# Kernel optimization log

Hardware: AMD Instinct MI355X
Metric: run time of the kernel (lower is better)

The kernel has to match this reference:

```python
import jax, jax.numpy as jnp
import numpy as np

B, C, N = 8, 256, 2048
NMOD = 5  # time, space, time_cor, space_cor, global_res


def _attn(x, y, Wqk, Vw, Vb, Tw, Tb):
    """Offset self-attention (PCT-style). x, y: [B, C, N].
    q/k share the same 1x1-conv weight Wqk; v and trans convs have bias.
    softmax over last axis, then L1 renorm over axis=1 of the [B,N,N] map.
    """
    x_q = jnp.einsum('oc,bcn->bno', Wqk, y)           # [B,N,C]
    x_k = jnp.einsum('oc,bcn->bon', Wqk, x)           # [B,C,N]
    x_v = jnp.einsum('oc,bcn->bon', Vw, x) + Vb[:, None]
    att = jax.nn.softmax(jnp.einsum('bnc,bcm->bnm', x_q, x_k), axis=-1)
    att = att / (1e-07 + att.sum(axis=1, keepdims=True))
    x_r = jnp.einsum('bcn,bnm->bcm', x_v, att)        # [B,C,N]
    x_r = jax.nn.relu(jnp.einsum('oc,bcn->bon', Tw, x - x_r) + Tb[:, None])
    return x + x_r


def setup_inputs() -> dict:
    key = jax.random.key(0)
    ks = jax.random.split(key, 6)
    s = 1.0 / np.sqrt(C)
    return {
        'x':   jax.random.normal(ks[0], (B, 3, C, N), dtype=jnp.float32),
        'Wqk': jax.random.normal(ks[1], (NMOD, C, C), dtype=jnp.float32) * s,
        'Vw':  jax.random.normal(ks[2], (NMOD, C, C), dtype=jnp.float32) * s,
        'Vb':  jax.random.normal(ks[3], (NMOD, C), dtype=jnp.float32) * s,
        'Tw':  jax.random.normal(ks[4], (NMOD, C, C), dtype=jnp.float32) * s,
        'Tb':  jax.random.normal(ks[5], (NMOD, C), dtype=jnp.float32) * s,
    }


def reference(x, Wqk, Vw, Vb, Tw, Tb):
    time_x, mid, space_x = x[:, 0], x[:, 1], x[:, 2]

    def A(i, xx, yy):
        return _attn(xx, yy, Wqk[i], Vw[i], Vb[i], Tw[i], Tb[i])

    time_att = A(0, time_x, time_x)
    space_att = A(1, space_x, space_x)
    time_cor = A(2, time_x, space_x)
    space_cor = A(3, space_x, time_x)
    global_feat = A(4, mid, mid)

    time_update = jnp.tanh(time_att * jax.nn.sigmoid(time_cor))
    space_update = jnp.tanh(space_att * jax.nn.sigmoid(space_cor))
    g_sig = jax.nn.sigmoid(global_feat)
    global_residual = jax.nn.sigmoid(time_update * g_sig + space_update * g_sig)
    return mid + global_residual * jnp.tanh(global_feat)
```

## Files before the change

kernel.cpp:

```cpp
#include <hip/hip_runtime.h>
#include <math.h>

#define BB 8
#define CC 256
#define NN 2048

static const size_t NC  = (size_t)NN * CC;
static const size_t CN  = (size_t)CC * NN;
static const size_t XBS = 3 * CN;

typedef unsigned short u16;
typedef __attribute__((ext_vector_type(8))) short short8;
typedef __attribute__((ext_vector_type(4))) float f32x4;

__device__ __forceinline__ float bf2f(u16 v) {
    union { unsigned int u; float f; } t; t.u = ((unsigned int)v) << 16; return t.f;
}
__device__ __forceinline__ u16 f2bf(float f) {
    union { float f; unsigned int u; } t; t.f = f;
    return (u16)((t.u + 0x7fffu + ((t.u >> 16) & 1u)) >> 16);
}
__device__ __forceinline__ float sigf(float x) { return 1.0f / (1.0f + expf(-x)); }

__device__ __forceinline__ size_t til(int r, int c, int tpr) {
    return (((size_t)((r >> 4) * tpr + (c >> 5))) << 9)
         + (size_t)((r & 15) << 5) + (size_t)(c & 31);
}

__global__ __launch_bounds__(256) void cast_w(const float* __restrict__ in,
                                              u16* __restrict__ outp)
{
    const int mat = blockIdx.y;
    const int idx = blockIdx.x * 256 + threadIdx.x;
    const int c = idx >> 6, k = (idx & 63) << 2;
    const float4 v = *(const float4*)&in[(size_t)mat * (CC * CC) + (size_t)c * CC + k];
    ushort4 p;
    p.x = f2bf(v.x); p.y = f2bf(v.y); p.z = f2bf(v.z); p.w = f2bf(v.w);
    *(ushort4*)&outp[(size_t)mat * (CC * CC) + til(c, k, CC / 32)] = p;
}

__global__ __launch_bounds__(256) void tcast_x(const float* __restrict__ in,
                                               u16* __restrict__ out)
{
    const int z = blockIdx.z;
    const float* I = in + (size_t)z * CN;
    u16* O = out + (size_t)z * NC;
    const int c0 = blockIdx.y * 64, n0 = blockIdx.x * 64;
    const int tx = threadIdx.x & 15, ty = threadIdx.x >> 4;

    __shared__ float t[64][68];

    #pragma unroll
    for (int cc = 0; cc < 64; cc += 16) {
        const int c = ty + cc;
        *(float4*)&t[c][tx * 4] = *(const float4*)&I[(size_t)(c0 + c) * NN + n0 + tx * 4];
    }
    __syncthreads();
    #pragma unroll
    for (int nn2 = 0; nn2 < 64; nn2 += 16) {
        const int n = n0 + ty + nn2;
        const int c = c0 + tx * 4;
        ushort4 p;
        p.x = f2bf(t[tx * 4 + 0][ty + nn2]);
        p.y = f2bf(t[tx * 4 + 1][ty + nn2]);
        p.z = f2bf(t[tx * 4 + 2][ty + nn2]);
        p.w = f2bf(t[tx * 4 + 3][ty + nn2]);
        *(ushort4*)&O[til(n, c, 8)] = p;
    }
}

struct QkvP {
    const u16* w[12]; const u16* x[12]; u16* out[12];
    const float* bias[12]; int isv[12];
};

__global__ __launch_bounds__(256) void conv_qkv(QkvP P)
{
    const int z = blockIdx.z, job = z >> 3, b = z & 7;
    const int isv = P.isv[job];
    const u16* Wp = P.w[job];
    const u16* Xp = P.x[job] + (size_t)b * (3 * NC);
    const int n0 = blockIdx.x * 128, c0 = blockIdx.y * 128;
    const int lane = threadIdx.x & 63, wave = threadIdx.x >> 6;
    const int l15 = lane & 15, lg = lane >> 4;
    const int rA = (wave >> 1) * 64, rB = (wave & 1) * 64;

    const u16* Ab = isv ? Xp : Wp;
    const u16* Bb = isv ? Wp : Xp;
    const int Ar0 = (isv ? n0 : c0) + rA;
    const int Br0 = (isv ? c0 : n0) + rB;

    const u16* ap[4]; const u16* bp[4];
    #pragma unroll
    for (int i = 0; i < 4; i++) {
        ap[i] = Ab + til(Ar0 + i * 16 + l15, lg * 8, 8);
        bp[i] = Bb + til(Br0 + i * 16 + l15, lg * 8, 8);
    }

    f32x4 acc[4][4] = {};
    #pragma unroll 2
    for (int kc = 0; kc < 8; kc++) {
        short8 av[4], bv[4];
        #pragma unroll
        for (int i = 0; i < 4; i++) av[i] = *(const short8*)(ap[i] + kc * 512);
        #pragma unroll
        for (int i = 0; i < 4; i++) bv[i] = *(const short8*)(bp[i] + kc * 512);
        #pragma unroll
        for (int i = 0; i < 4; i++)
            #pragma unroll
            for (int j = 0; j < 4; j++)
                acc[i][j] = __builtin_amdgcn_mfma_f32_16x16x32_bf16(av[i], bv[j], acc[i][j], 0, 0, 0);
    }

    if (!isv) {
        u16* Ot = P.out[job] + (size_t)b * NC;
        #pragma unroll
        for (int i = 0; i < 4; i++) {
            const int c = c0 + rA + i * 16 + lg * 4;
            #pragma unroll
            for (int j = 0; j < 4; j++) {
                const int n = n0 + rB + j * 16 + l15;
                ushort4 p;
                p.x = f2bf(acc[i][j][0]); p.y = f2bf(acc[i][j][1]);
                p.z = f2bf(acc[i][j][2]); p.w = f2bf(acc[i][j][3]);
                *(ushort4*)&Ot[til(n, c, 8)] = p;
            }
        }
    } else {
        u16* Ov = P.out[job] + (size_t)b * CN;
        const float* bias = P.bias[job];
        #pragma unroll
        for (int j = 0; j < 4; j++) {
            const int c = c0 + rB + j * 16 + l15;
            const float bi = bias[c];
            #pragma unroll
            for (int i = 0; i < 4; i++) {
                const int n = n0 + rA + i * 16 + lg * 4;
                ushort4 p;
                p.x = f2bf(acc[i][j][0] + bi); p.y = f2bf(acc[i][j][1] + bi);
                p.z = f2bf(acc[i][j][2] + bi); p.w = f2bf(acc[i][j][3] + bi);
                *(ushort4*)&Ov[til(c, n, 64)] = p;
            }
        }
    }
}

__global__ __launch_bounds__(256) void conv_t(
    const u16* __restrict__ W, const u16* __restrict__ Dt,
    const float* __restrict__ bias, const float* __restrict__ xsrc,
    float* __restrict__ Ofull)
{
    const int b = blockIdx.z;
    const u16* Xp = Dt + (size_t)b * NC;
    const int n0 = blockIdx.x * 128, c0 = blockIdx.y * 128;
    const int lane = threadIdx.x & 63, wave = threadIdx.x >> 6;
    const int l15 = lane & 15, lg = lane >> 4;
    const int wc = (wave >> 1) * 64, wn = (wave & 1) * 64;

    const u16* ap[4]; const u16* bp[4];
    #pragma unroll
    for (int i = 0; i < 4; i++) {
        ap[i] = W  + til(c0 + wc + i * 16 + l15, lg * 8, 8);
        bp[i] = Xp + til(n0 + wn + i * 16 + l15, lg * 8, 8);
    }

    f32x4 acc[4][4] = {};
    #pragma unroll 2
    for (int kc = 0; kc < 8; kc++) {
        short8 av[4], bv[4];
        #pragma unroll
        for (int i = 0; i < 4; i++) av[i] = *(const short8*)(ap[i] + kc * 512);
        #pragma unroll
        for (int i = 0; i < 4; i++) bv[i] = *(const short8*)(bp[i] + kc * 512);
        #pragma unroll
        for (int i = 0; i < 4; i++)
            #pragma unroll
            for (int j = 0; j < 4; j++)
                acc[i][j] = __builtin_amdgcn_mfma_f32_16x16x32_bf16(av[i], bv[j], acc[i][j], 0, 0, 0);
    }

    float* Of = Ofull + (size_t)b * CN;
    const float* Xr = xsrc + (size_t)b * XBS;
    #pragma unroll
    for (int i = 0; i < 4; i++)
        #pragma unroll
        for (int r = 0; r < 4; r++) {
            const int c = c0 + wc + i * 16 + lg * 4 + r;
            const float bi = bias[c];
            #pragma unroll
            for (int j = 0; j < 4; j++) {
                const int n = n0 + wn + j * 16 + l15;
                Of[(size_t)c * NN + n] = Xr[(size_t)c * NN + n] + fmaxf(acc[i][j][r] + bi, 0.0f);
            }
        }
}

__global__ __launch_bounds__(1024) void attn_mfma4(
    const u16* __restrict__ Q, const u16* __restrict__ K,
    u16* __restrict__ Sout, float* __restrict__ CPb)
{
    const int bid = blockIdx.x;
    const int b = bid & 7;
    const int nblk = bid >> 3;
    const int n0 = nblk * 32;
    const int tid = threadIdx.x, lane = tid & 63, wave = tid >> 6;
    const int l15 = lane & 15, lg = lane >> 4;

    const u16* Qt = Q + (size_t)b * NC;
    const u16* Kt = K + (size_t)b * NC;

    f32x4 acc[2][8];
    #pragma unroll
    for (int g = 0; g < 2; g++)
        #pragma unroll
        for (int t = 0; t < 8; t++) acc[g][t] = (f32x4){0.f, 0.f, 0.f, 0.f};

    const u16* qb0 = Qt + til(n0 + l15,      lg * 8, 8);
    const u16* qb1 = Qt + til(n0 + 16 + l15, lg * 8, 8);
    const u16* kb  = Kt + til(wave * 128 + l15, lg * 8, 8);

    #pragma unroll
    for (int kc = 0; kc < 8; kc++) {
        const short8 a0 = *(const short8*)(qb0 + kc * 512);
        const short8 a1 = *(const short8*)(qb1 + kc * 512);
        short8 bf[8];
        #pragma unroll
        for (int t = 0; t < 8; t++)
            bf[t] = *(const short8*)(kb + t * 4096 + kc * 512);
        #pragma unroll
        for (int t = 0; t < 8; t++) {
            acc[0][t] = __builtin_amdgcn_mfma_f32_16x16x32_bf16(a0, bf[t], acc[0][t], 0, 0, 0);
            acc[1][t] = __builtin_amdgcn_mfma_f32_16x16x32_bf16(a1, bf[t], acc[1][t], 0, 0, 0);
        }
    }

    __shared__ float red[16][32];
    __shared__ float rowstat[32];

    float pm[2][4];
    #pragma unroll
    for (int g = 0; g < 2; g++)
        #pragma unroll
        for (int r = 0; r < 4; r++) {
            float m = acc[g][0][r];
            #pragma unroll
            for (int t = 1; t < 8; t++) m = fmaxf(m, acc[g][t][r]);
            #pragma unroll
            for (int o = 1; o <= 8; o <<= 1) m = fmaxf(m, __shfl_xor(m, o));
            pm[g][r] = m;
        }
    if (l15 == 0) {
        #pragma unroll
        for (int g = 0; g < 2; g++)
            #pragma unroll
            for (int r = 0; r < 4; r++) red[wave][g * 16 + lg * 4 + r] = pm[g][r];
    }
    __syncthreads();
    if (tid < 32) {
        float m = red[0][tid];
        #pragma unroll
        for (int w = 1; w < 16; w++) m = fmaxf(m, red[w][tid]);
        rowstat[tid] = m;
    }
    __syncthreads();

    float rm[2][4], ps[2][4];
    #pragma unroll
    for (int g = 0; g < 2; g++)
        #pragma unroll
        for (int r = 0; r < 4; r++) { rm[g][r] = rowstat[g * 16 + lg * 4 + r]; ps[g][r] = 0.f; }
    __syncthreads();

    #pragma unroll
    for (int g = 0; g < 2; g++)
        #pragma unroll
        for (int t = 0; t < 8; t++)
            #pragma unroll
            for (int r = 0; r < 4; r++) {
                const float e = __expf(acc[g][t][r] - rm[g][r]);
                acc[g][t][r] = e; ps[g][r] += e;
            }
    #pragma unroll
    for (int g = 0; g < 2; g++)
        #pragma unroll
        for (int r = 0; r < 4; r++)
            #pragma unroll
            for (int o = 1; o <= 8; o <<= 1) ps[g][r] += __shfl_xor(ps[g][r], o);
    if (l15 == 0) {
        #pragma unroll
        for (int g = 0; g < 2; g++)
            #pragma unroll
            for (int r = 0; r < 4; r++) red[wave][g * 16 + lg * 4 + r] = ps[g][r];
    }
    __syncthreads();
    if (tid < 32) {
        float s = red[0][tid];
        #pragma unroll
        for (int w = 1; w < 16; w++) s += red[w][tid];
        rowstat[tid] = 1.0f / s;
    }
    __syncthreads();

    float rv[2][4];
    #pragma unroll
    for (int g = 0; g < 2; g++)
        #pragma unroll
        for (int r = 0; r < 4; r++) rv[g][r] = rowstat[g * 16 + lg * 4 + r];

    u16* sb = Sout + (size_t)b * NN * NN;
    u16* sbg[2];
    #pragma unroll
    for (int g = 0; g < 2; g++)
        sbg[g] = sb + (size_t)((n0 >> 3) + g * 2 + (lg >> 1)) * (NN * 8) + (lg & 1) * 4;
    float* cpb = CPb + ((size_t)b * 64 + nblk) * NN;

    #pragma unroll
    for (int t = 0; t < 8; t++) {
        const int m = wave * 128 + t * 16 + l15;
        float cs = 0.0f;
        #pragma unroll
        for (int g = 0; g < 2; g++) {
            const float v0 = acc[g][t][0] * rv[g][0], v1 = acc[g][t][1] * rv[g][1];
            const float v2 = acc[g][t][2] * rv[g][2], v3 = acc[g][t][3] * rv[g][3];
            ushort4 pk;
            pk.x = f2bf(v0); pk.y = f2bf(v1); pk.z = f2bf(v2); pk.w = f2bf(v3);
            *(ushort4*)&sbg[g][(size_t)m * 8] = pk;
            cs += v0 + v1 + v2 + v3;
        }
        cs += __shfl_xor(cs, 16);
        cs += __shfl_xor(cs, 32);
        if (lane < 16) cpb[m] = cs;
    }
}

__global__ __launch_bounds__(256) void csum_kernel(const float* __restrict__ cp,
                                                   float* __restrict__ cs)
{
    const int b  = blockIdx.y;
    const int ml = threadIdx.x & 63;
    const int m  = blockIdx.x * 64 + ml;
    const int g0 = threadIdx.x >> 6;
    float s = 0.0f;
    for (int g = g0; g < 64; g += 4)
        s += cp[((size_t)b * 64 + g) * NN + m];
    __shared__ float red[4][64];
    red[g0][ml] = s;
    __syncthreads();
    if (threadIdx.x < 64) {
        cs[(size_t)b * NN + blockIdx.x * 64 + threadIdx.x] =
            red[0][threadIdx.x] + red[1][threadIdx.x] +
            red[2][threadIdx.x] + red[3][threadIdx.x];
    }
}

__global__ __launch_bounds__(256) void pv_mfma(
    const u16* __restrict__ V, const u16* __restrict__ S,
    const float* __restrict__ CSb, const u16* __restrict__ Xts,
    u16* __restrict__ DTo)
{
    const int bid = blockIdx.x;
    const int b = bid & 7;
    const int r2 = bid >> 3;
    const int cy = r2 & 1, mx = r2 >> 1;
    const int m0b = mx * 64, c0 = cy * 128;
    const int lane = threadIdx.x & 63, wave = threadIdx.x >> 6;
    const int wc = (wave >> 1) * 64, wm = (wave & 1) * 32;
    const int l15 = lane & 15, lg = lane >> 4;

    const u16* Vm = V + (size_t)b * CN;
    const u16* Sm = S + (size_t)b * NN * NN;

    f32x4 acc[4][2] = {};
    const u16* vp[4]; const u16* sp[2];
    #pragma unroll
    for (int ai = 0; ai < 4; ai++)
        vp[ai] = Vm + til(c0 + wc + ai * 16 + l15, lg * 8, 64);
    #pragma unroll
    for (int bj = 0; bj < 2; bj++)
        sp[bj] = Sm + ((size_t)lg * NN + m0b + wm + bj * 16 + l15) * 8;

    #pragma unroll 2
    for (int kc = 0; kc < 64; kc++) {
        short8 a[4], s2[2];
        #pragma unroll
        for (int ai = 0; ai < 4; ai++) { a[ai] = *(const short8*)vp[ai]; vp[ai] += 512; }
        #pragma unroll
        for (int bj = 0; bj < 2; bj++) { s2[bj] = *(const short8*)sp[bj]; sp[bj] += (size_t)4 * NN * 8; }
        #pragma unroll
        for (int ai = 0; ai < 4; ai++)
            #pragma unroll
            for (int bj = 0; bj < 2; bj++)
                acc[ai][bj] = __builtin_amdgcn_mfma_f32_16x16x32_bf16(a[ai], s2[bj], acc[ai][bj], 0, 0, 0);
    }

    const u16* Xtb = Xts + (size_t)b * (3 * NC);
    u16* Dtb = DTo + (size_t)b * NC;

    #pragma unroll
    for (int bj = 0; bj < 2; bj++) {
        const int m = m0b + wm + bj * 16 + l15;
        const float inv = 1.0f / (1e-7f + CSb[(size_t)b * NN + m]);
        #pragma unroll
        for (int ai = 0; ai < 4; ai++) {
            const int c = c0 + wc + ai * 16 + lg * 4;
            const size_t ad = til(m, c, 8);
            const ushort4 xv = *(const ushort4*)&Xtb[ad];
            ushort4 pk;
            pk.x = f2bf(bf2f(xv.x) - acc[ai][bj][0] * inv);
            pk.y = f2bf(bf2f(xv.y) - acc[ai][bj][1] * inv);
            pk.z = f2bf(bf2f(xv.z) - acc[ai][bj][2] * inv);
            pk.w = f2bf(bf2f(xv.w) - acc[ai][bj][3] * inv);
            *(ushort4*)&Dtb[ad] = pk;
        }
    }
}

__global__ __launch_bounds__(256) void ew_update_kernel(float* __restrict__ A,
                                                        const float* __restrict__ Bv)
{
    const size_t i = ((size_t)blockIdx.x * 256 + threadIdx.x) * 4;
    float4 a = *(float4*)&A[i];
    const float4 b = *(const float4*)&Bv[i];
    a.x = tanhf(a.x * sigf(b.x));
    a.y = tanhf(a.y * sigf(b.y));
    a.z = tanhf(a.z * sigf(b.z));
    a.w = tanhf(a.w * sigf(b.w));
    *(float4*)&A[i] = a;
}

__global__ __launch_bounds__(256) void ew_final_kernel(const float* __restrict__ TU,
                                                       const float* __restrict__ SU,
                                                       const float* __restrict__ x,
                                                       float* __restrict__ OUT)
{
    const size_t i   = ((size_t)blockIdx.x * 256 + threadIdx.x) * 4;
    const size_t b   = i / CN;
    const size_t off = i - b * CN;
    const float4 mid = *(const float4*)&x[(b * 3 + 1) * CN + off];
    const float4 g   = *(const float4*)&OUT[i];
    const float4 tu  = *(const float4*)&TU[i];
    const float4 su  = *(const float4*)&SU[i];
    float4 o;
    o.x = mid.x + sigf((tu.x + su.x) * sigf(g.x)) * tanhf(g.x);
    o.y = mid.y + sigf((tu.y + su.y) * sigf(g.y)) * tanhf(g.y);
    o.z = mid.z + sigf((tu.z + su.z) * sigf(g.z)) * tanhf(g.z);
    o.w = mid.w + sigf((tu.w + su.w) * sigf(g.w)) * tanhf(g.w);
    *(float4*)&OUT[i] = o;
}

extern "C" void kernel_launch(void* const* d_in, const int* in_sizes, int n_in,
                              void* d_out, int out_size, void* d_ws, size_t ws_size,
                              hipStream_t stream)
{
    const float* x   = (const float*)d_in[0];
    const float* Wqk = (const float*)d_in[1];
    const float* Vw  = (const float*)d_in[2];
    const float* VbF = (const float*)d_in[3];
    const float* Tw  = (const float*)d_in[4];
    const float* TbF = (const float*)d_in[5];
    float* out = (float*)d_out;

    const int mxs[5] = {0, 2, 0, 2, 1};
    const int mys[5] = {0, 2, 2, 0, 1};
    const int qjob[5] = {0, 1, 5, 6, 4};
    const int q_wi[7] = {0, 1, 2, 3, 4, 2, 3};
    const int q_xi[7] = {0, 2, 0, 2, 1, 2, 0};

    const size_t WSZ     = (size_t)CC * CC;
    const size_t QK_SLAB = (size_t)BB * NC;
    const size_t S_SLAB  = (size_t)BB * NN * NN;
    const size_t CP_SLAB = (size_t)BB * 64 * NN;
    const size_t CS_SLAB = (size_t)BB * NN;
    const size_t O_SLAB  = (size_t)BB * CN;

    const size_t base_b = 15 * WSZ * 2 + (size_t)BB * 3 * NC * 2;
    const size_t mod_b  = S_SLAB * 2 + CP_SLAB * 4 + CS_SLAB * 4 + QK_SLAB * 2 ;
    const size_t margin = 2u << 20;
    const size_t need_1 = base_b + 12 * QK_SLAB * 2 + mod_b + 2 * O_SLAB * 4 + margin;
    const size_t need_2 = base_b +  3 * QK_SLAB * 2 + mod_b + 2 * O_SLAB * 4 + margin;

    const int tier = (ws_size >= need_1) ? 1 : 2;
    if (tier == 2 && ws_size < need_2) return;

    const int nQK = (tier == 1) ? 7 : 2;
    const int nV  = (tier == 1) ? 5 : 1;

    char* ws = (char*)d_ws;
    size_t off = 0;
    auto alloc = [&](size_t bytes) -> char* {
        char* p = ws + off; off += (bytes + 255) & ~255ULL; return p;
    };

    u16*   W16 = (u16*)  alloc(15 * WSZ * 2);
    u16*   Xt  = (u16*)  alloc((size_t)BB * 3 * NC * 2);
    u16*   QK  = (u16*)  alloc((size_t)nQK * QK_SLAB * 2);
    u16*   VB  = (u16*)  alloc((size_t)nV * QK_SLAB * 2);
    u16*   S   = (u16*)  alloc(S_SLAB * 2);
    float* CP  = (float*)alloc(CP_SLAB * 4);
    float* CS  = (float*)alloc(CS_SLAB * 4);
    u16*   DT  = (u16*)  alloc(QK_SLAB * 2);
    float* OB  = (float*)alloc(2 * O_SLAB * 4);

    cast_w<<<dim3(64, 5), 256, 0, stream>>>(Wqk, W16);
    cast_w<<<dim3(64, 5), 256, 0, stream>>>(Vw,  W16 + 5 * WSZ);
    cast_w<<<dim3(64, 5), 256, 0, stream>>>(Tw,  W16 + 10 * WSZ);
    tcast_x<<<dim3(NN / 64, CC / 64, BB * 3), 256, 0, stream>>>(x, Xt);

    if (tier == 1) {
        QkvP qp{};
        for (int j = 0; j < 7; j++) {
            qp.w[j] = W16 + (size_t)q_wi[j] * WSZ;
            qp.x[j] = Xt + (size_t)q_xi[j] * NC;
            qp.out[j] = QK + (size_t)j * QK_SLAB;
            qp.isv[j] = 0; qp.bias[j] = nullptr;
        }
        for (int i = 0; i < 5; i++) {
            const int j = 7 + i;
            qp.w[j] = W16 + (size_t)(5 + i) * WSZ;
            qp.x[j] = Xt + (size_t)mxs[i] * NC;
            qp.out[j] = VB + (size_t)i * QK_SLAB;
            qp.isv[j] = 1; qp.bias[j] = VbF + (size_t)i * CC;
        }
        conv_qkv<<<dim3(NN / 128, CC / 128, 96), 256, 0, stream>>>(qp);
    }

    auto run_mod = [&](int i, float* O) {
        const u16* Qp; const u16* Kp; const u16* Vp;
        if (tier == 1) {
            Qp = QK + (size_t)qjob[i] * QK_SLAB;
            Kp = QK + (size_t)i * QK_SLAB;
            Vp = VB + (size_t)i * QK_SLAB;
        } else {
            QkvP qp{}; int nj = 0;
            qp.w[nj] = W16 + (size_t)i * WSZ; qp.x[nj] = Xt + (size_t)mxs[i] * NC;
            qp.out[nj] = QK; qp.isv[nj] = 0; nj++;
            Qp = QK; Kp = QK;
            if (mys[i] != mxs[i]) {
                qp.w[nj] = W16 + (size_t)i * WSZ; qp.x[nj] = Xt + (size_t)mys[i] * NC;
                qp.out[nj] = QK + QK_SLAB; qp.isv[nj] = 0; nj++;
                Qp = QK + QK_SLAB;
            }
            qp.w[nj] = W16 + (size_t)(5 + i) * WSZ; qp.x[nj] = Xt + (size_t)mxs[i] * NC;
            qp.out[nj] = VB; qp.isv[nj] = 1; qp.bias[nj] = VbF + (size_t)i * CC; nj++;
            conv_qkv<<<dim3(NN / 128, CC / 128, 8 * nj), 256, 0, stream>>>(qp);
            Vp = VB;
        }
        attn_mfma4<<<512, 1024, 0, stream>>>(Qp, Kp, S, CP);
        csum_kernel<<<dim3(NN / 64, BB), 256, 0, stream>>>(CP, CS);
        pv_mfma<<<512, 256, 0, stream>>>(Vp, S, CS, Xt + (size_t)mxs[i] * NC, DT);
        conv_t<<<dim3(NN / 128, CC / 128, BB), 256, 0, stream>>>(
            W16 + (size_t)(10 + i) * WSZ, DT, TbF + (size_t)i * CC,
            x + (size_t)mxs[i] * CN, O);
    };

    run_mod(0, OB);
    run_mod(2, OB + O_SLAB);
    ew_update_kernel<<<4096, 256, 0, stream>>>(OB, OB + O_SLAB);
    run_mod(1, OB + O_SLAB);
    run_mod(3, out);
    ew_update_kernel<<<4096, 256, 0, stream>>>(OB + O_SLAB, out);
    run_mod(4, out);
    ew_final_kernel<<<4096, 256, 0, stream>>>(OB, OB + O_SLAB, x, out);
}
```

Baseline: 773.0 us.

## Batch attention tail across modules and fold column-sum into PV kernel

Attention, PV and output-conv kernels now take per-module pointer tables so up to five modules run in a single launch each, with workspace sized to hold several S/CP/DT slabs. The separate column-sum kernel is removed; each PV block reduces the partial column sums for its 64 columns itself. The aim is fewer launches and more blocks per launch to fill the GPU. In exchange it needs much more workspace, and each PV block re-reads the column partials redundantly. The final elementwise combine is reordered to use four output buffers.

New measurement: 808.1 us. 4.5% more time.

```diff
diff --git a/kernel.cpp b/kernel.cpp
--- a/kernel.cpp
+++ b/kernel.cpp
@@ -145,13 +145,16 @@
     }
 }
 
-__global__ __launch_bounds__(256) void conv_t(
-    const u16* __restrict__ W, const u16* __restrict__ Dt,
-    const float* __restrict__ bias, const float* __restrict__ xsrc,
-    float* __restrict__ Ofull)
-{
-    const int b = blockIdx.z;
-    const u16* Xp = Dt + (size_t)b * NC;
+struct TcvP {
+    const u16* w[5]; const u16* dt[5]; const float* bias[5];
+    const float* xsrc[5]; float* o[5];
+};
+
+__global__ __launch_bounds__(256) void conv_t(TcvP P)
+{
+    const int z = blockIdx.z, mod = z >> 3, b = z & 7;
+    const u16* W  = P.w[mod];
+    const u16* Xp = P.dt[mod] + (size_t)b * NC;
     const int n0 = blockIdx.x * 128, c0 = blockIdx.y * 128;
     const int lane = threadIdx.x & 63, wave = threadIdx.x >> 6;
     const int l15 = lane & 15, lg = lane >> 4;
@@ -179,8 +182,9 @@
                 acc[i][j] = __builtin_amdgcn_mfma_f32_16x16x32_bf16(av[i], bv[j], acc[i][j], 0, 0, 0);
     }
 
-    float* Of = Ofull + (size_t)b * CN;
-    const float* Xr = xsrc + (size_t)b * XBS;
+    float* Of = P.o[mod] + (size_t)b * CN;
+    const float* Xr = P.xsrc[mod] + (size_t)b * XBS;
+    const float* bias = P.bias[mod];
     #pragma unroll
     for (int i = 0; i < 4; i++)
         #pragma unroll
@@ -195,19 +199,21 @@
         }
 }
 
-__global__ __launch_bounds__(1024) void attn_mfma4(
-    const u16* __restrict__ Q, const u16* __restrict__ K,
-    u16* __restrict__ Sout, float* __restrict__ CPb)
+struct AttnP { const u16* q[5]; const u16* k[5]; u16* s[5]; float* cp[5]; };
+
+__global__ __launch_bounds__(1024) void attn_mfma5(AttnP P)
 {
     const int bid = blockIdx.x;
-    const int b = bid & 7;
-    const int nblk = bid >> 3;
+    const int mod = bid >> 9;
+    const int within = bid & 511;
+    const int b = within & 7;
+    const int nblk = within >> 3;
     const int n0 = nblk * 32;
     const int tid = threadIdx.x, lane = tid & 63, wave = tid >> 6;
     const int l15 = lane & 15, lg = lane >> 4;
 
-    const u16* Qt = Q + (size_t)b * NC;
-    const u16* Kt = K + (size_t)b * NC;
+    const u16* Qt = P.q[mod] + (size_t)b * NC;
+    const u16* Kt = P.k[mod] + (size_t)b * NC;
 
     f32x4 acc[2][8];
     #pragma unroll
@@ -307,12 +313,12 @@
         #pragma unroll
         for (int r = 0; r < 4; r++) rv[g][r] = rowstat[g * 16 + lg * 4 + r];
 
-    u16* sb = Sout + (size_t)b * NN * NN;
+    u16* sb = P.s[mod] + (size_t)b * NN * NN;
     u16* sbg[2];
     #pragma unroll
     for (int g = 0; g < 2; g++)
         sbg[g] = sb + (size_t)((n0 >> 3) + g * 2 + (lg >> 1)) * (NN * 8) + (lg & 1) * 4;
-    float* cpb = CPb + ((size_t)b * 64 + nblk) * NN;
+    float* cpb = P.cp[mod] + ((size_t)b * 64 + nblk) * NN;
 
     #pragma unroll
     for (int t = 0; t < 8; t++) {
@@ -333,42 +339,42 @@
     }
 }
 
-__global__ __launch_bounds__(256) void csum_kernel(const float* __restrict__ cp,
-                                                   float* __restrict__ cs)
-{
-    const int b  = blockIdx.y;
-    const int ml = threadIdx.x & 63;
-    const int m  = blockIdx.x * 64 + ml;
-    const int g0 = threadIdx.x >> 6;
-    float s = 0.0f;
-    for (int g = g0; g < 64; g += 4)
-        s += cp[((size_t)b * 64 + g) * NN + m];
-    __shared__ float red[4][64];
-    red[g0][ml] = s;
-    __syncthreads();
-    if (threadIdx.x < 64) {
-        cs[(size_t)b * NN + blockIdx.x * 64 + threadIdx.x] =
-            red[0][threadIdx.x] + red[1][threadIdx.x] +
-            red[2][threadIdx.x] + red[3][threadIdx.x];
-    }
-}
-
-__global__ __launch_bounds__(256) void pv_mfma(
-    const u16* __restrict__ V, const u16* __restrict__ S,
-    const float* __restrict__ CSb, const u16* __restrict__ Xts,
-    u16* __restrict__ DTo)
+struct PvP { const u16* v[5]; const u16* s[5]; const float* cp[5];
+             const u16* xt[5]; u16* dt[5]; };
+
+__global__ __launch_bounds__(256) void pv_mfma2(PvP P)
 {
     const int bid = blockIdx.x;
-    const int b = bid & 7;
-    const int r2 = bid >> 3;
+    const int mod = bid >> 9;
+    const int within = bid & 511;
+    const int b = within & 7;
+    const int r2 = within >> 3;
     const int cy = r2 & 1, mx = r2 >> 1;
     const int m0b = mx * 64, c0 = cy * 128;
-    const int lane = threadIdx.x & 63, wave = threadIdx.x >> 6;
+    const int tid = threadIdx.x;
+    const int lane = tid & 63, wave = tid >> 6;
     const int wc = (wave >> 1) * 64, wm = (wave & 1) * 32;
     const int l15 = lane & 15, lg = lane >> 4;
 
-    const u16* Vm = V + (size_t)b * CN;
-    const u16* Sm = S + (size_t)b * NN * NN;
+    __shared__ float redcs[4][64];
+    __shared__ float csl[64];
+    {
+        const float* CPm = P.cp[mod];
+        const int mloc = tid & 63, gq = tid >> 6;
+        float s = 0.0f;
+        #pragma unroll
+        for (int j = 0; j < 16; j++)
+            s += CPm[((size_t)b * 64 + gq + j * 4) * NN + m0b + mloc];
+        redcs[gq][mloc] = s;
+    }
+    __syncthreads();
+    if (tid < 64)
+        csl[tid] = 1.0f / (1e-7f + redcs[0][tid] + redcs[1][tid] +
+                           redcs[2][tid] + redcs[3][tid]);
+    __syncthreads();
+
+    const u16* Vm = P.v[mod] + (size_t)b * CN;
+    const u16* Sm = P.s[mod] + (size_t)b * NN * NN;
 
     f32x4 acc[4][2] = {};
     const u16* vp[4]; const u16* sp[2];
@@ -393,13 +399,14 @@
                 acc[ai][bj] = __builtin_amdgcn_mfma_f32_16x16x32_bf16(a[ai], s2[bj], acc[ai][bj], 0, 0, 0);
     }
 
-    const u16* Xtb = Xts + (size_t)b * (3 * NC);
-    u16* Dtb = DTo + (size_t)b * NC;
+    const u16* Xtb = P.xt[mod] + (size_t)b * (3 * NC);
+    u16* Dtb = P.dt[mod] + (size_t)b * NC;
 
     #pragma unroll
     for (int bj = 0; bj < 2; bj++) {
-        const int m = m0b + wm + bj * 16 + l15;
-        const float inv = 1.0f / (1e-7f + CSb[(size_t)b * NN + m]);
+        const int ml = wm + bj * 16 + l15;
+        const int m = m0b + ml;
+        const float inv = csl[ml];
         #pragma unroll
         for (int ai = 0; ai < 4; ai++) {
             const int c = c0 + wc + ai * 16 + lg * 4;
@@ -470,20 +477,30 @@
     const size_t QK_SLAB = (size_t)BB * NC;
     const size_t S_SLAB  = (size_t)BB * NN * NN;
     const size_t CP_SLAB = (size_t)BB * 64 * NN;
-    const size_t CS_SLAB = (size_t)BB * NN;
     const size_t O_SLAB  = (size_t)BB * CN;
 
     const size_t base_b = 15 * WSZ * 2 + (size_t)BB * 3 * NC * 2;
-    const size_t mod_b  = S_SLAB * 2 + CP_SLAB * 4 + CS_SLAB * 4 + QK_SLAB * 2 ;
+    const size_t modtl  = S_SLAB * 2 + CP_SLAB * 4 + QK_SLAB * 2;
     const size_t margin = 2u << 20;
-    const size_t need_1 = base_b + 12 * QK_SLAB * 2 + mod_b + 2 * O_SLAB * 4 + margin;
-    const size_t need_2 = base_b +  3 * QK_SLAB * 2 + mod_b + 2 * O_SLAB * 4 + margin;
-
-    const int tier = (ws_size >= need_1) ? 1 : 2;
-    if (tier == 2 && ws_size < need_2) return;
-
-    const int nQK = (tier == 1) ? 7 : 2;
-    const int nV  = (tier == 1) ? 5 : 1;
+
+    auto need = [&](int g, int nqkv, int nob) {
+        return base_b + (size_t)nqkv * QK_SLAB * 2 + (size_t)g * modtl
+             + (size_t)nob * O_SLAB * 4 + margin;
+    };
+
+    int g = 0;
+    for (int cand = 5; cand >= 2; cand--)
+        if (ws_size >= need(cand, 12, 4)) { g = cand; break; }
+    int tier2 = 0;
+    if (!g) {
+        if (ws_size >= need(1, 12, 2)) g = 1;
+        else if (ws_size >= need(1, 3, 2)) { g = 1; tier2 = 1; }
+        else return;
+    }
+
+    const int nQK = tier2 ? 2 : 7;
+    const int nV  = tier2 ? 1 : 5;
+    const int nOB = (g == 1) ? 2 : 4;
 
     char* ws = (char*)d_ws;
     size_t off = 0;
@@ -495,18 +512,17 @@
     u16*   Xt  = (u16*)  alloc((size_t)BB * 3 * NC * 2);
     u16*   QK  = (u16*)  alloc((size_t)nQK * QK_SLAB * 2);
     u16*   VB  = (u16*)  alloc((size_t)nV * QK_SLAB * 2);
-    u16*   S   = (u16*)  alloc(S_SLAB * 2);
-    float* CP  = (float*)alloc(CP_SLAB * 4);
-    float* CS  = (float*)alloc(CS_SLAB * 4);
-    u16*   DT  = (u16*)  alloc(QK_SLAB * 2);
-    float* OB  = (float*)alloc(2 * O_SLAB * 4);
+    u16*   S   = (u16*)  alloc((size_t)g * S_SLAB * 2);
+    float* CP  = (float*)alloc((size_t)g * CP_SLAB * 4);
+    u16*   DT  = (u16*)  alloc((size_t)g * QK_SLAB * 2);
+    float* OB  = (float*)alloc((size_t)nOB * O_SLAB * 4);
 
     cast_w<<<dim3(64, 5), 256, 0, stream>>>(Wqk, W16);
     cast_w<<<dim3(64, 5), 256, 0, stream>>>(Vw,  W16 + 5 * WSZ);
     cast_w<<<dim3(64, 5), 256, 0, stream>>>(Tw,  W16 + 10 * WSZ);
     tcast_x<<<dim3(NN / 64, CC / 64, BB * 3), 256, 0, stream>>>(x, Xt);
 
-    if (tier == 1) {
+    if (!tier2) {
         QkvP qp{};
         for (int j = 0; j < 7; j++) {
             qp.w[j] = W16 + (size_t)q_wi[j] * WSZ;
@@ -524,9 +540,51 @@
         conv_qkv<<<dim3(NN / 128, CC / 128, 96), 256, 0, stream>>>(qp);
     }
 
+    auto run_tail = [&](int m0, int nm,
+                        const u16* const* qv, const u16* const* kv,
+                        const u16* const* vv, float* const* ov) {
+        AttnP ap{}; PvP pp{}; TcvP tv{};
+        for (int j = 0; j < nm; j++) {
+            const int i = m0 + j;
+            ap.q[j] = qv[j]; ap.k[j] = kv[j];
+            ap.s[j] = S + (size_t)j * S_SLAB;
+            ap.cp[j] = CP + (size_t)j * CP_SLAB;
+            pp.v[j] = vv[j]; pp.s[j] = ap.s[j]; pp.cp[j] = ap.cp[j];
+            pp.xt[j] = Xt + (size_t)mxs[i] * NC;
+            pp.dt[j] = DT + (size_t)j * QK_SLAB;
+            tv.w[j] = W16 + (size_t)(10 + i) * WSZ;
+            tv.dt[j] = pp.dt[j];
+            tv.bias[j] = TbF + (size_t)i * CC;
+            tv.xsrc[j] = x + (size_t)mxs[i] * CN;
+            tv.o[j] = ov[j];
+        }
+        attn_mfma5<<<dim3(nm * 512), 1024, 0, stream>>>(ap);
+        pv_mfma2<<<dim3(nm * 512), 256, 0, stream>>>(pp);
+        conv_t<<<dim3(NN / 128, CC / 128, 8 * nm), 256, 0, stream>>>(tv);
+    };
+
+    if (g >= 2) {
+        for (int m0 = 0; m0 < 5; m0 += g) {
+            const int nm = (5 - m0 < g) ? (5 - m0) : g;
+            const u16* qv[5]; const u16* kv[5]; const u16* vv[5]; float* ov[5];
+            for (int j = 0; j < nm; j++) {
+                const int i = m0 + j;
+                qv[j] = QK + (size_t)qjob[i] * QK_SLAB;
+                kv[j] = QK + (size_t)i * QK_SLAB;
+                vv[j] = VB + (size_t)i * QK_SLAB;
+                ov[j] = (i < 4) ? (OB + (size_t)i * O_SLAB) : out;
+            }
+            run_tail(m0, nm, qv, kv, vv, ov);
+        }
+        ew_update_kernel<<<4096, 256, 0, stream>>>(OB + 0 * O_SLAB, OB + 2 * O_SLAB);
+        ew_update_kernel<<<4096, 256, 0, stream>>>(OB + 1 * O_SLAB, OB + 3 * O_SLAB);
+        ew_final_kernel<<<4096, 256, 0, stream>>>(OB + 0 * O_SLAB, OB + 1 * O_SLAB, x, out);
+        return;
+    }
+
     auto run_mod = [&](int i, float* O) {
         const u16* Qp; const u16* Kp; const u16* Vp;
-        if (tier == 1) {
+        if (!tier2) {
             Qp = QK + (size_t)qjob[i] * QK_SLAB;
             Kp = QK + (size_t)i * QK_SLAB;
             Vp = VB + (size_t)i * QK_SLAB;
@@ -545,12 +603,9 @@
             conv_qkv<<<dim3(NN / 128, CC / 128, 8 * nj), 256, 0, stream>>>(qp);
             Vp = VB;
         }
-        attn_mfma4<<<512, 1024, 0, stream>>>(Qp, Kp, S, CP);
-        csum_kernel<<<dim3(NN / 64, BB), 256, 0, stream>>>(CP, CS);
-        pv_mfma<<<512, 256, 0, stream>>>(Vp, S, CS, Xt + (size_t)mxs[i] * NC, DT);
-        conv_t<<<dim3(NN / 128, CC / 128, BB), 256, 0, stream>>>(
-            W16 + (size_t)(10 + i) * WSZ, DT, TbF + (size_t)i * CC,
-            x + (size_t)mxs[i] * CN, O);
+        const u16* qv[1] = {Qp}; const u16* kv[1] = {Kp};
+        const u16* vv[1] = {Vp}; float* ov[1] = {O};
+        run_tail(i, 1, qv, kv, vv, ov);
     };
 
     run_mod(0, OB);
```

## Store module outputs as tiled bf16 and read residual from bf16 input

Applied to the files above, without the earlier changes.

The output projection kernel now writes its result as bf16 in a tiled layout instead of fp32 row-major, and reads the residual from the already-transposed bf16 input copy rather than the fp32 input. The elementwise update and final kernels work on bf16 tiled buffers, and the final kernel de-tiles while writing the fp32 output. The grid launch is flattened with batch as the fastest-varying index. This cuts intermediate memory traffic roughly in half, at the cost of extra bf16 rounding on intermediates and residuals, plus scattered 2-byte stores in the conv epilogue.

Measured after the change: 709.8 us. 1.09x faster.

```diff
diff --git a/kernel.cpp b/kernel.cpp
--- a/kernel.cpp
+++ b/kernel.cpp
@@ -7,7 +7,6 @@
 
 static const size_t NC  = (size_t)NN * CC;
 static const size_t CN  = (size_t)CC * NN;
-static const size_t XBS = 3 * CN;
 
 typedef unsigned short u16;
 typedef __attribute__((ext_vector_type(8))) short short8;
@@ -145,18 +144,21 @@
     }
 }
 
-__global__ __launch_bounds__(256) void conv_t(
+__global__ __launch_bounds__(256) void conv_t2(
     const u16* __restrict__ W, const u16* __restrict__ Dt,
-    const float* __restrict__ bias, const float* __restrict__ xsrc,
-    float* __restrict__ Ofull)
-{
-    const int b = blockIdx.z;
-    const u16* Xp = Dt + (size_t)b * NC;
-    const int n0 = blockIdx.x * 128, c0 = blockIdx.y * 128;
+    const float* __restrict__ bias, const u16* __restrict__ Xts,
+    u16* __restrict__ O)
+{
+    const int bid = blockIdx.x;
+    const int b = bid & 7;
+    const int rest = bid >> 3;
+    const int cy = rest & 1, nx = rest >> 1;
+    const int n0 = nx * 128, c0 = cy * 128;
     const int lane = threadIdx.x & 63, wave = threadIdx.x >> 6;
     const int l15 = lane & 15, lg = lane >> 4;
     const int wc = (wave >> 1) * 64, wn = (wave & 1) * 64;
 
+    const u16* Xp = Dt + (size_t)b * NC;
     const u16* ap[4]; const u16* bp[4];
     #pragma unroll
     for (int i = 0; i < 4; i++) {
@@ -179,20 +181,24 @@
                 acc[i][j] = __builtin_amdgcn_mfma_f32_16x16x32_bf16(av[i], bv[j], acc[i][j], 0, 0, 0);
     }
 
-    float* Of = Ofull + (size_t)b * CN;
-    const float* Xr = xsrc + (size_t)b * XBS;
-    #pragma unroll
-    for (int i = 0; i < 4; i++)
-        #pragma unroll
-        for (int r = 0; r < 4; r++) {
-            const int c = c0 + wc + i * 16 + lg * 4 + r;
-            const float bi = bias[c];
-            #pragma unroll
-            for (int j = 0; j < 4; j++) {
-                const int n = n0 + wn + j * 16 + l15;
-                Of[(size_t)c * NN + n] = Xr[(size_t)c * NN + n] + fmaxf(acc[i][j][r] + bi, 0.0f);
+    const u16* Xtb = Xts + (size_t)b * (3 * NC);
+    u16* Ob = O + (size_t)b * CN;
+    #pragma unroll
+    for (int i = 0; i < 4; i++) {
+        const int cb = c0 + wc + i * 16 + lg * 4;
+        #pragma unroll
+        for (int j = 0; j < 4; j++) {
+            const int n = n0 + wn + j * 16 + l15;
+            const ushort4 xv = *(const ushort4*)&Xtb[til(n, cb, 8)];
+            const u16 xa[4] = { xv.x, xv.y, xv.z, xv.w };
+            #pragma unroll
+            for (int r = 0; r < 4; r++) {
+                const int c = cb + r;
+                const float v = bf2f(xa[r]) + fmaxf(acc[i][j][r] + bias[c], 0.0f);
+                Ob[til(c, n, 64)] = f2bf(v);
             }
         }
+    }
 }
 
 __global__ __launch_bounds__(1024) void attn_mfma4(
@@ -415,37 +421,51 @@
     }
 }
 
-__global__ __launch_bounds__(256) void ew_update_kernel(float* __restrict__ A,
-                                                        const float* __restrict__ Bv)
-{
-    const size_t i = ((size_t)blockIdx.x * 256 + threadIdx.x) * 4;
-    float4 a = *(float4*)&A[i];
-    const float4 b = *(const float4*)&Bv[i];
-    a.x = tanhf(a.x * sigf(b.x));
-    a.y = tanhf(a.y * sigf(b.y));
-    a.z = tanhf(a.z * sigf(b.z));
-    a.w = tanhf(a.w * sigf(b.w));
-    *(float4*)&A[i] = a;
-}
-
-__global__ __launch_bounds__(256) void ew_final_kernel(const float* __restrict__ TU,
-                                                       const float* __restrict__ SU,
-                                                       const float* __restrict__ x,
-                                                       float* __restrict__ OUT)
-{
-    const size_t i   = ((size_t)blockIdx.x * 256 + threadIdx.x) * 4;
-    const size_t b   = i / CN;
-    const size_t off = i - b * CN;
-    const float4 mid = *(const float4*)&x[(b * 3 + 1) * CN + off];
-    const float4 g   = *(const float4*)&OUT[i];
-    const float4 tu  = *(const float4*)&TU[i];
-    const float4 su  = *(const float4*)&SU[i];
-    float4 o;
-    o.x = mid.x + sigf((tu.x + su.x) * sigf(g.x)) * tanhf(g.x);
-    o.y = mid.y + sigf((tu.y + su.y) * sigf(g.y)) * tanhf(g.y);
-    o.z = mid.z + sigf((tu.z + su.z) * sigf(g.z)) * tanhf(g.z);
-    o.w = mid.w + sigf((tu.w + su.w) * sigf(g.w)) * tanhf(g.w);
-    *(float4*)&OUT[i] = o;
+__global__ __launch_bounds__(256) void ew_update_t(u16* __restrict__ A,
+                                                   const u16* __restrict__ Bv)
+{
+    const size_t e = ((size_t)blockIdx.x * 256 + threadIdx.x) * 8;
+    short8 a = *(const short8*)&A[e];
+    const short8 b = *(const short8*)&Bv[e];
+    #pragma unroll
+    for (int j = 0; j < 8; j++) {
+        const float f = tanhf(bf2f((u16)a[j]) * sigf(bf2f((u16)b[j])));
+        a[j] = (short)f2bf(f);
+    }
+    *(short8*)&A[e] = a;
+}
+
+__global__ __launch_bounds__(256) void ew_final_t(
+    const u16* __restrict__ TU, const u16* __restrict__ SU,
+    const u16* __restrict__ G, const float* __restrict__ x,
+    float* __restrict__ OUT)
+{
+    const size_t e = ((size_t)blockIdx.x * 256 + threadIdx.x) * 8;
+    const int b = (int)(e / CN);
+    const size_t r = e - (size_t)b * CN;
+    const int tile = (int)(r >> 9), win = (int)(r & 511);
+    const int row = win >> 5, col = win & 31;
+    const int c = (tile >> 6) * 16 + row;
+    const int n = (tile & 63) * 32 + col;
+
+    const size_t lin = ((size_t)b * 3 + 1) * CN + (size_t)c * NN + n;
+    const float4 m0 = *(const float4*)&x[lin];
+    const float4 m1 = *(const float4*)&x[lin + 4];
+    const float mid[8] = { m0.x, m0.y, m0.z, m0.w, m1.x, m1.y, m1.z, m1.w };
+
+    const short8 tu = *(const short8*)&TU[e];
+    const short8 su = *(const short8*)&SU[e];
+    const short8 g  = *(const short8*)&G[e];
+
+    float o[8];
+    #pragma unroll
+    for (int j = 0; j < 8; j++) {
+        const float gg = bf2f((u16)g[j]);
+        o[j] = mid[j] + sigf((bf2f((u16)tu[j]) + bf2f((u16)su[j])) * sigf(gg)) * tanhf(gg);
+    }
+    float* op = OUT + (size_t)b * CN + (size_t)c * NN + n;
+    *(float4*)op       = (float4){o[0], o[1], o[2], o[3]};
+    *(float4*)(op + 4) = (float4){o[4], o[5], o[6], o[7]};
 }
 
 extern "C" void kernel_launch(void* const* d_in, const int* in_sizes, int n_in,
@@ -474,16 +494,16 @@
     const size_t O_SLAB  = (size_t)BB * CN;
 
     const size_t base_b = 15 * WSZ * 2 + (size_t)BB * 3 * NC * 2;
-    const size_t mod_b  = S_SLAB * 2 + CP_SLAB * 4 + CS_SLAB * 4 + QK_SLAB * 2 ;
+    const size_t modtl  = S_SLAB * 2 + CP_SLAB * 4 + CS_SLAB * 4 + QK_SLAB * 2;
     const size_t margin = 2u << 20;
-    const size_t need_1 = base_b + 12 * QK_SLAB * 2 + mod_b + 2 * O_SLAB * 4 + margin;
-    const size_t need_2 = base_b +  3 * QK_SLAB * 2 + mod_b + 2 * O_SLAB * 4 + margin;
-
-    const int tier = (ws_size >= need_1) ? 1 : 2;
-    if (tier == 2 && ws_size < need_2) return;
-
-    const int nQK = (tier == 1) ? 7 : 2;
-    const int nV  = (tier == 1) ? 5 : 1;
+    const size_t need_1 = base_b + 12 * QK_SLAB * 2 + modtl + 3 * O_SLAB * 2 + margin;
+    const size_t need_2 = base_b +  3 * QK_SLAB * 2 + modtl + 3 * O_SLAB * 2 + margin;
+
+    const int tier2 = (ws_size >= need_1) ? 0 : 1;
+    if (tier2 && ws_size < need_2) return;
+
+    const int nQK = tier2 ? 2 : 7;
+    const int nV  = tier2 ? 1 : 5;
 
     char* ws = (char*)d_ws;
     size_t off = 0;
@@ -499,14 +519,14 @@
     float* CP  = (float*)alloc(CP_SLAB * 4);
     float* CS  = (float*)alloc(CS_SLAB * 4);
     u16*   DT  = (u16*)  alloc(QK_SLAB * 2);
-    float* OB  = (float*)alloc(2 * O_SLAB * 4);
+    u16*   OB  = (u16*)  alloc(3 * O_SLAB * 2);
 
     cast_w<<<dim3(64, 5), 256, 0, stream>>>(Wqk, W16);
     cast_w<<<dim3(64, 5), 256, 0, stream>>>(Vw,  W16 + 5 * WSZ);
     cast_w<<<dim3(64, 5), 256, 0, stream>>>(Tw,  W16 + 10 * WSZ);
     tcast_x<<<dim3(NN / 64, CC / 64, BB * 3), 256, 0, stream>>>(x, Xt);
 
-    if (tier == 1) {
+    if (!tier2) {
         QkvP qp{};
         for (int j = 0; j < 7; j++) {
             qp.w[j] = W16 + (size_t)q_wi[j] * WSZ;
@@ -524,9 +544,9 @@
         conv_qkv<<<dim3(NN / 128, CC / 128, 96), 256, 0, stream>>>(qp);
     }
 
-    auto run_mod = [&](int i, float* O) {
+    auto run_mod = [&](int i, u16* O) {
         const u16* Qp; const u16* Kp; const u16* Vp;
-        if (tier == 1) {
+        if (!tier2) {
             Qp = QK + (size_t)qjob[i] * QK_SLAB;
             Kp = QK + (size_t)i * QK_SLAB;
             Vp = VB + (size_t)i * QK_SLAB;
@@ -548,17 +568,22 @@
         attn_mfma4<<<512, 1024, 0, stream>>>(Qp, Kp, S, CP);
         csum_kernel<<<dim3(NN / 64, BB), 256, 0, stream>>>(CP, CS);
         pv_mfma<<<512, 256, 0, stream>>>(Vp, S, CS, Xt + (size_t)mxs[i] * NC, DT);
-        conv_t<<<dim3(NN / 128, CC / 128, BB), 256, 0, stream>>>(
-            W16 + (size_t)(10 + i) * WSZ, DT, TbF + (size_t)i * CC,
-            x + (size_t)mxs[i] * CN, O);
+        conv_t2<<<256, 256, 0, stream>>>(W16 + (size_t)(10 + i) * WSZ, DT,
+                                         TbF + (size_t)i * CC,
+                                         Xt + (size_t)mxs[i] * NC, O);
     };
 
-    run_mod(0, OB);
-    run_mod(2, OB + O_SLAB);
-    ew_update_kernel<<<4096, 256, 0, stream>>>(OB, OB + O_SLAB);
-    run_mod(1, OB + O_SLAB);
-    run_mod(3, out);
-    ew_update_kernel<<<4096, 256, 0, stream>>>(OB + O_SLAB, out);
-    run_mod(4, out);
-    ew_final_kernel<<<4096, 256, 0, stream>>>(OB, OB + O_SLAB, x, out);
-}
+    u16* OB0 = OB;
+    u16* OB1 = OB + O_SLAB;
+    u16* OB2 = OB + 2 * O_SLAB;
+    const int ewg = (int)(((size_t)BB * CN) / (256 * 8));
+
+    run_mod(0, OB0);
+    run_mod(2, OB1);
+    ew_update_t<<<ewg, 256, 0, stream>>>(OB0, OB1);
+    run_mod(1, OB1);
+    run_mod(3, OB2);
+    ew_update_t<<<ewg, 256, 0, stream>>>(OB1, OB2);
+    run_mod(4, OB2);
+    ew_final_t<<<ewg, 256, 0, stream>>>(OB0, OB1, OB2, x, out);
+}
```
